# Performance work log

Hardware: AMD Instinct MI355X
Metric: run time of the kernel (lower is better)

Reference implementation:

```python
import jax, jax.numpy as jnp
import numpy as np

B, S, D_IN, D_OUT = 4, 2048, 4096, 11008


def setup_inputs() -> dict:
    key = jax.random.key(0)
    k1, k2, k3 = jax.random.split(key, 3)
    x = jax.random.normal(k1, (B, S, D_IN), dtype=jnp.float32)
    # ternary weights in {-1, 0, +1}, stored as int8 (as the torch buffer does)
    quantized_weight = (jax.random.randint(k2, (D_OUT, D_IN), 0, 3) - 1).astype(jnp.int8)
    weight_scale = jnp.ones((1,), dtype=jnp.float32) * 0.02  # mean-abs scale
    bias = jax.random.normal(k3, (D_OUT,), dtype=jnp.float32) * 0.01
    return {"x": x, "quantized_weight": quantized_weight,
            "weight_scale": weight_scale, "bias": bias}


def reference(x, quantized_weight, weight_scale, bias):
    # Dequantize: ternary int8 -> float, times scalar scale (matches
    # weight = self.quantized_weight.float() * self.weight_scale)
    w = quantized_weight.astype(jnp.float32) * weight_scale[0]
    # F.linear: y = x @ w.T + bias ; x: (B,S,D_in), w: (D_out,D_in)
    out = jnp.einsum("bsd,od->bso", x, w) + bias
    return out
```

## Files before the change

kernel.cpp:

```cpp
#include <hip/hip_runtime.h>
#include <stdint.h>

#define M_DIM 8192
#define N_DIM 11008
#define K_DIM 4096

#define BM 256
#define BN 256
#define BK 128
#define KTILES (K_DIM / BK)

#define FBM 128
#define FBN 128

typedef __attribute__((ext_vector_type(4))) int i32x4;
typedef __attribute__((ext_vector_type(8))) short bf16x8;
typedef __attribute__((ext_vector_type(4))) float f32x4;

__device__ __forceinline__ void async_cp16(const void* g, void* lds_uniform) {
  __builtin_amdgcn_global_load_lds(
      (__attribute__((address_space(1))) void*)(uintptr_t)g,
      (__attribute__((address_space(3))) void*)(uintptr_t)lds_uniform,
      16, 0, 0);
}

__device__ __forceinline__ unsigned short f2bf(float f) {
  unsigned int u = __float_as_uint(f);
  u += 0x7fffu + ((u >> 16) & 1u);
  return (unsigned short)(u >> 16);
}
__device__ __forceinline__ unsigned short i2bf(int v) {
  return (unsigned short)(__float_as_uint((float)v) >> 16);
}

__device__ __forceinline__ int pack4(int a, int b, int c, int d) {
  return (a & 0xFF) | ((b & 0xFF) << 8) | ((c & 0xFF) << 16) | ((d & 0xFF) << 24);
}

__global__ __launch_bounds__(256) void quant_x(const float* __restrict__ x,
                                               signed char* __restrict__ xq,
                                               float* __restrict__ row_step) {
  __shared__ float red[256];
  const unsigned int row = blockIdx.x, t = threadIdx.x;
  const float* xr = x + (size_t)row * K_DIM;
  float4 v[4];
#pragma unroll
  for (int j = 0; j < 4; ++j)
    v[j] = *(const float4*)(xr + j * 1024 + t * 4);

  float m = 0.f;
#pragma unroll
  for (int j = 0; j < 4; ++j) {
    m = fmaxf(m, fmaxf(fmaxf(fabsf(v[j].x), fabsf(v[j].y)),
                       fmaxf(fabsf(v[j].z), fabsf(v[j].w))));
  }
  red[t] = m;
  __syncthreads();
#pragma unroll
  for (int s = 128; s > 0; s >>= 1) {
    if (t < s) red[t] = fmaxf(red[t], red[t + s]);
    __syncthreads();
  }
  const float mx = red[0];
  const float r = (mx > 0.f) ? 127.0f / mx : 0.0f;
  if (t == 0) row_step[row] = (mx > 0.f) ? mx / 127.0f : 0.0f;

  int* out = (int*)(xq + (size_t)row * K_DIM);
#pragma unroll
  for (int j = 0; j < 4; ++j) {
    int q0 = __float2int_rn(v[j].x * r);
    int q1 = __float2int_rn(v[j].y * r);
    int q2 = __float2int_rn(v[j].z * r);
    int q3 = __float2int_rn(v[j].w * r);
    out[j * 256 + t] = pack4(q0, q1, q2, q3);
  }
}

__global__ __launch_bounds__(256) void quant_w(const int4* __restrict__ w,
                                               int* __restrict__ wq) {
  const size_t base = (size_t)blockIdx.x * 1024 + threadIdx.x;
#pragma unroll
  for (int j = 0; j < 4; ++j) {
    int4 a = w[base + j * 256];
    wq[base + j * 256] = pack4(a.x, a.y, a.z, a.w);
  }
}

__device__ __forceinline__ void ktile_iter(
    const signed char* Ab, const signed char* Bb,
    signed char* An, signed char* Bn, bool pf,
    i32x4 (&acc)[8][4],
    const signed char* (&ag)[4], const signed char* (&bg)[4],
    unsigned abase, unsigned bbase, unsigned ldsw)
{
  i32x4 bfr[4][2];
#pragma unroll
  for (int ni = 0; ni < 4; ++ni)
#pragma unroll
    for (int ks = 0; ks < 2; ++ks)
      bfr[ni][ks] = *(const i32x4*)(Bb + ((bbase + ni * 2048u) ^ (unsigned)(ks << 6)));

  i32x4 afr[2][2];

#pragma unroll
  for (int mi = 0; mi < 2; ++mi)
#pragma unroll
    for (int ks = 0; ks < 2; ++ks)
      afr[mi][ks] = *(const i32x4*)(Ab + ((abase + mi * 2048u) ^ (unsigned)(ks << 6)));
  if (pf) {
    async_cp16(ag[0], An + 0 * 8192 + ldsw);
    async_cp16(ag[1], An + 1 * 8192 + ldsw);
    async_cp16(bg[0], Bn + 0 * 8192 + ldsw);
    async_cp16(bg[1], Bn + 1 * 8192 + ldsw);
  }
  __builtin_amdgcn_s_barrier();
  asm volatile("s_waitcnt lgkmcnt(0)" ::: "memory");
  __builtin_amdgcn_sched_barrier(0);
  __builtin_amdgcn_s_setprio(1);
#pragma unroll
  for (int mi = 0; mi < 2; ++mi)
#pragma unroll
    for (int ni = 0; ni < 4; ++ni)
#pragma unroll
      for (int ks = 0; ks < 2; ++ks)
        acc[mi][ni] = __builtin_amdgcn_mfma_i32_16x16x64_i8(afr[mi][ks], bfr[ni][ks], acc[mi][ni], 0, 0, 0);
  __builtin_amdgcn_s_setprio(0);
  __builtin_amdgcn_s_barrier();

#pragma unroll
  for (int mi = 0; mi < 2; ++mi)
#pragma unroll
    for (int ks = 0; ks < 2; ++ks)
      afr[mi][ks] = *(const i32x4*)(Ab + ((abase + (mi + 2) * 2048u) ^ (unsigned)(ks << 6)));
  if (pf) {
    async_cp16(ag[2], An + 2 * 8192 + ldsw);
    async_cp16(ag[3], An + 3 * 8192 + ldsw);
    async_cp16(bg[2], Bn + 2 * 8192 + ldsw);
    async_cp16(bg[3], Bn + 3 * 8192 + ldsw);
  }
  __builtin_amdgcn_s_barrier();
  asm volatile("s_waitcnt lgkmcnt(0)" ::: "memory");
  __builtin_amdgcn_sched_barrier(0);
  __builtin_amdgcn_s_setprio(1);
#pragma unroll
  for (int mi = 0; mi < 2; ++mi)
#pragma unroll
    for (int ni = 0; ni < 4; ++ni)
#pragma unroll
      for (int ks = 0; ks < 2; ++ks)
        acc[mi + 2][ni] = __builtin_amdgcn_mfma_i32_16x16x64_i8(afr[mi][ks], bfr[ni][ks], acc[mi + 2][ni], 0, 0, 0);
  __builtin_amdgcn_s_setprio(0);
  __builtin_amdgcn_s_barrier();

#pragma unroll
  for (int mi = 0; mi < 2; ++mi)
#pragma unroll
    for (int ks = 0; ks < 2; ++ks)
      afr[mi][ks] = *(const i32x4*)(Ab + ((abase + (mi + 4) * 2048u) ^ (unsigned)(ks << 6)));
  __builtin_amdgcn_s_barrier();
  asm volatile("s_waitcnt lgkmcnt(0)" ::: "memory");
  __builtin_amdgcn_sched_barrier(0);
  __builtin_amdgcn_s_setprio(1);
#pragma unroll
  for (int mi = 0; mi < 2; ++mi)
#pragma unroll
    for (int ni = 0; ni < 4; ++ni)
#pragma unroll
      for (int ks = 0; ks < 2; ++ks)
        acc[mi + 4][ni] = __builtin_amdgcn_mfma_i32_16x16x64_i8(afr[mi][ks], bfr[ni][ks], acc[mi + 4][ni], 0, 0, 0);
  __builtin_amdgcn_s_setprio(0);
  __builtin_amdgcn_s_barrier();

#pragma unroll
  for (int mi = 0; mi < 2; ++mi)
#pragma unroll
    for (int ks = 0; ks < 2; ++ks)
      afr[mi][ks] = *(const i32x4*)(Ab + ((abase + (mi + 6) * 2048u) ^ (unsigned)(ks << 6)));
  __builtin_amdgcn_s_barrier();
  asm volatile("s_waitcnt lgkmcnt(0)" ::: "memory");
  __builtin_amdgcn_sched_barrier(0);
  __builtin_amdgcn_s_setprio(1);
#pragma unroll
  for (int mi = 0; mi < 2; ++mi)
#pragma unroll
    for (int ni = 0; ni < 4; ++ni)
#pragma unroll
      for (int ks = 0; ks < 2; ++ks)
        acc[mi + 6][ni] = __builtin_amdgcn_mfma_i32_16x16x64_i8(afr[mi][ks], bfr[ni][ks], acc[mi + 6][ni], 0, 0, 0);
  __builtin_amdgcn_s_setprio(0);
  asm volatile("s_waitcnt vmcnt(0)" ::: "memory");
  __builtin_amdgcn_s_barrier();

#pragma unroll
  for (int g = 0; g < 4; ++g) { ag[g] += BK; bg[g] += BK; }
}

__global__ __launch_bounds__(512, 2) void gemm_i8(
    const signed char* __restrict__ A,
    const signed char* __restrict__ B,
    const float* __restrict__ row_step,
    const float* __restrict__ bias,
    const float* __restrict__ scale_p,
    float* __restrict__ C)
{
  __shared__ __align__(16) signed char As[2][BM * BK];
  __shared__ __align__(16) signed char Bs[2][BN * BK];

  const unsigned t = threadIdx.x;
  const unsigned lane = t & 63u;
  const unsigned wave = t >> 6;
  const unsigned n0 = blockIdx.x * BN;
  const unsigned m0 = blockIdx.y * BM;

  const unsigned wm = (wave >> 2) * 128u;
  const unsigned wn = (wave & 3u) * 64u;
  const unsigned fr = lane & 15u;
  const unsigned fq = lane >> 4;

  const unsigned rst = t >> 3;
  const unsigned cst = (lane & 7u) ^ ((lane >> 3) & 7u);
  const signed char* ag[4];
  const signed char* bg[4];
#pragma unroll
  for (int g = 0; g < 4; ++g) {
    ag[g] = A + (size_t)(m0 + g * 64 + rst) * K_DIM + cst * 16u;
    bg[g] = B + (size_t)(n0 + g * 64 + rst) * K_DIM + cst * 16u;
  }
  const unsigned ldsw = wave * 1024u;

  const unsigned swz = ((fq ^ (fr & 3u)) << 4) | (((fr >> 2) & 1u) << 6);
  const unsigned abase = (wm + fr) * BK + swz;
  const unsigned bbase = (wn + fr) * BK + swz;

  i32x4 acc[8][4];
#pragma unroll
  for (int i = 0; i < 8; ++i)
#pragma unroll
    for (int j = 0; j < 4; ++j)
      acc[i][j] = (i32x4){0, 0, 0, 0};

#pragma unroll
  for (int g = 0; g < 4; ++g) {
    async_cp16(ag[g], As[0] + g * 8192 + ldsw);
    async_cp16(bg[g], Bs[0] + g * 8192 + ldsw);
    ag[g] += BK; bg[g] += BK;
  }
  asm volatile("s_waitcnt vmcnt(0)" ::: "memory");
  __builtin_amdgcn_s_barrier();

  for (int kt = 0; kt < KTILES; kt += 2) {
    ktile_iter(As[0], Bs[0], As[1], Bs[1], true,
               acc, ag, bg, abase, bbase, ldsw);
    ktile_iter(As[1], Bs[1], As[0], Bs[0], (kt + 2) < KTILES,
               acc, ag, bg, abase, bbase, ldsw);
  }

  const float ws = scale_p[0];
  float bb[4];
#pragma unroll
  for (int ni = 0; ni < 4; ++ni)
    bb[ni] = bias[n0 + wn + ni * 16 + fr];

#pragma unroll
  for (int mi = 0; mi < 8; ++mi) {
    const unsigned mg = m0 + wm + mi * 16 + fq * 4;
    const float rs0 = row_step[mg + 0] * ws;
    const float rs1 = row_step[mg + 1] * ws;
    const float rs2 = row_step[mg + 2] * ws;
    const float rs3 = row_step[mg + 3] * ws;
#pragma unroll
    for (int ni = 0; ni < 4; ++ni) {
      const unsigned ng = n0 + wn + ni * 16 + fr;
      i32x4 v = acc[mi][ni];
      float* cp = C + (size_t)mg * N_DIM + ng;
      cp[0]                   = (float)v[0] * rs0 + bb[ni];
      cp[(size_t)1 * N_DIM]   = (float)v[1] * rs1 + bb[ni];
      cp[(size_t)2 * N_DIM]   = (float)v[2] * rs2 + bb[ni];
      cp[(size_t)3 * N_DIM]   = (float)v[3] * rs3 + bb[ni];
    }
  }
}

__global__ __launch_bounds__(256) void gemm_fused(
    const float* __restrict__ X,
    const int* __restrict__ W,
    const float* __restrict__ bias,
    const float* __restrict__ scale_p,
    float* __restrict__ C)
{
  __shared__ __align__(16) unsigned short As[FBM * 32];
  __shared__ __align__(16) unsigned short Bs[FBN * 32];

  const unsigned int t = threadIdx.x;
  const unsigned int n0 = blockIdx.x * FBN;
  const unsigned int m0 = blockIdx.y * FBM;
  const unsigned int lane = t & 63u;
  const unsigned int wave = t >> 6;
  const unsigned int wm = (wave >> 1) * 64u;
  const unsigned int wn = (wave & 1u) * 64u;
  const unsigned int fr = lane & 15u;
  const unsigned int fq = lane >> 4;

  const unsigned short* afp = As + (wm + fr) * 32 + fq * 8u;
  const unsigned short* bfp = Bs + (wn + fr) * 32 + fq * 8u;
  const unsigned int brow = t >> 1, bcol = (t & 1u) * 16u;

  f32x4 acc[4][4];
#pragma unroll
  for (int i = 0; i < 4; ++i)
#pragma unroll
    for (int j = 0; j < 4; ++j)
      acc[i][j] = (f32x4){0.f, 0.f, 0.f, 0.f};

  for (int kt = 0; kt < K_DIM; kt += 32) {
#pragma unroll
    for (int i = 0; i < 4; ++i) {
      unsigned int c = t + i * 256;
      unsigned int row = c >> 3, col = (c & 7u) * 4u;
      float4 v = *(const float4*)(X + (size_t)(m0 + row) * K_DIM + kt + col);
      ushort4 o;
      o.x = f2bf(v.x); o.y = f2bf(v.y); o.z = f2bf(v.z); o.w = f2bf(v.w);
      *(ushort4*)(As + row * 32 + col) = o;
    }
    {
      const int* wp = W + (size_t)(n0 + brow) * K_DIM + kt + bcol;
      int4 a = *(const int4*)(wp);
      int4 b = *(const int4*)(wp + 4);
      int4 c = *(const int4*)(wp + 8);
      int4 d = *(const int4*)(wp + 12);
      uint4 o0, o1;
      o0.x = (unsigned int)i2bf(a.x) | ((unsigned int)i2bf(a.y) << 16);
      o0.y = (unsigned int)i2bf(a.z) | ((unsigned int)i2bf(a.w) << 16);
      o0.z = (unsigned int)i2bf(b.x) | ((unsigned int)i2bf(b.y) << 16);
      o0.w = (unsigned int)i2bf(b.z) | ((unsigned int)i2bf(b.w) << 16);
      o1.x = (unsigned int)i2bf(c.x) | ((unsigned int)i2bf(c.y) << 16);
      o1.y = (unsigned int)i2bf(c.z) | ((unsigned int)i2bf(c.w) << 16);
      o1.z = (unsigned int)i2bf(d.x) | ((unsigned int)i2bf(d.y) << 16);
      o1.w = (unsigned int)i2bf(d.z) | ((unsigned int)i2bf(d.w) << 16);
      *(uint4*)(Bs + brow * 32 + bcol)     = o0;
      *(uint4*)(Bs + brow * 32 + bcol + 8) = o1;
    }
    __syncthreads();

    bf16x8 af[4], bgf[4];
#pragma unroll
    for (int mi = 0; mi < 4; ++mi)
      af[mi] = *(const bf16x8*)(afp + mi * 16 * 32);
#pragma unroll
    for (int ni = 0; ni < 4; ++ni)
      bgf[ni] = *(const bf16x8*)(bfp + ni * 16 * 32);
#pragma unroll
    for (int mi = 0; mi < 4; ++mi)
#pragma unroll
      for (int ni = 0; ni < 4; ++ni)
        acc[mi][ni] = __builtin_amdgcn_mfma_f32_16x16x32_bf16(af[mi], bgf[ni], acc[mi][ni], 0, 0, 0);
    __syncthreads();
  }

  const float scale = scale_p[0];
#pragma unroll
  for (int ni = 0; ni < 4; ++ni) {
    const unsigned int ng = n0 + wn + ni * 16 + fr;
    const float bbv = bias[ng];
#pragma unroll
    for (int mi = 0; mi < 4; ++mi) {
      const unsigned int mg = m0 + wm + mi * 16 + fq * 4;
      f32x4 v = acc[mi][ni];
#pragma unroll
      for (int r = 0; r < 4; ++r)
        C[(size_t)(mg + r) * N_DIM + ng] = v[r] * scale + bbv;
    }
  }
}

extern "C" void kernel_launch(void* const* d_in, const int* in_sizes, int n_in,
                              void* d_out, int out_size, void* d_ws, size_t ws_size,
                              hipStream_t stream) {
  const float* x     = (const float*)d_in[0];
  const int*   wq    = (const int*)d_in[1];
  const float* scale = (const float*)d_in[2];
  const float* bias  = (const float*)d_in[3];
  float* out         = (float*)d_out;

  const size_t xq_bytes = (size_t)M_DIM * K_DIM;
  const size_t wq_bytes = (size_t)N_DIM * K_DIM;
  const size_t rs_bytes = (size_t)M_DIM * sizeof(float);
  const size_t need = xq_bytes + wq_bytes + rs_bytes;

  if (ws_size >= need) {
    signed char* xqp = (signed char*)d_ws;
    signed char* wqp = xqp + xq_bytes;
    float* row_step  = (float*)(wqp + wq_bytes);

    dim3 grid(N_DIM / BN, M_DIM / BM);
    quant_x<<<M_DIM, 256, 0, stream>>>(x, xqp, row_step);
    quant_w<<<(unsigned)(wq_bytes / (16 * 256)), 256, 0, stream>>>(
        (const int4*)wq, (int*)wqp);
    gemm_i8<<<grid, 512, 0, stream>>>(xqp, wqp, row_step, bias, scale, out);
  } else {
    dim3 fgrid(N_DIM / FBN, M_DIM / FBM);
    gemm_fused<<<fgrid, 256, 0, stream>>>(x, wq, bias, scale, out);
  }
}
```

Baseline: 903.6 us.

## Shrink int8 GEMM tiles, raise occupancy, add XCD block remap and nontemporal stores

Reduces the int8 GEMM block tile from 256x256x128 to 256x128x64, with each of 8 waves computing a 64x64 sub-tile. The LDS XOR swizzle and global-to-LDS copy mapping are reworked to match, and launch bounds now ask for 4 blocks per CU. The aim is more resident blocks to hide latency, and fewer registers because the accumulator is half the size. Block ids are remapped so neighbouring tiles are grouped per XCD, which should improve L2 reuse. Output stores become nontemporal. The trade-offs are lower arithmetic intensity per block and twice as many k-iterations with barriers. LDS demand may also still cap occupancy below the requested 4 blocks.

```diff
diff --git a/kernel.cpp b/kernel.cpp
--- a/kernel.cpp
+++ b/kernel.cpp
@@ -6,8 +6,8 @@
 #define K_DIM 4096
 
 #define BM 256
-#define BN 256
-#define BK 128
+#define BN 128
+#define BK 64
 #define KTILES (K_DIM / BK)
 
 #define FBM 128
@@ -89,29 +89,24 @@
 __device__ __forceinline__ void ktile_iter(
     const signed char* Ab, const signed char* Bb,
     signed char* An, signed char* Bn, bool pf,
-    i32x4 (&acc)[8][4],
-    const signed char* (&ag)[4], const signed char* (&bg)[4],
+    i32x4 (&acc)[4][4],
+    const signed char*& ag0, const signed char*& ag1, const signed char*& bg0,
     unsigned abase, unsigned bbase, unsigned ldsw)
 {
-  i32x4 bfr[4][2];
+  i32x4 bfr[4];
 #pragma unroll
   for (int ni = 0; ni < 4; ++ni)
-#pragma unroll
-    for (int ks = 0; ks < 2; ++ks)
-      bfr[ni][ks] = *(const i32x4*)(Bb + ((bbase + ni * 2048u) ^ (unsigned)(ks << 6)));
-
-  i32x4 afr[2][2];
+    bfr[ni] = *(const i32x4*)(Bb + bbase + ni * 1024u);
+
+  i32x4 afr[2];
 
 #pragma unroll
   for (int mi = 0; mi < 2; ++mi)
-#pragma unroll
-    for (int ks = 0; ks < 2; ++ks)
-      afr[mi][ks] = *(const i32x4*)(Ab + ((abase + mi * 2048u) ^ (unsigned)(ks << 6)));
+    afr[mi] = *(const i32x4*)(Ab + abase + mi * 1024u);
   if (pf) {
-    async_cp16(ag[0], An + 0 * 8192 + ldsw);
-    async_cp16(ag[1], An + 1 * 8192 + ldsw);
-    async_cp16(bg[0], Bn + 0 * 8192 + ldsw);
-    async_cp16(bg[1], Bn + 1 * 8192 + ldsw);
+    async_cp16(ag0, An + ldsw);
+    async_cp16(ag1, An + 8192 + ldsw);
+    async_cp16(bg0, Bn + ldsw);
   }
   __builtin_amdgcn_s_barrier();
   asm volatile("s_waitcnt lgkmcnt(0)" ::: "memory");
@@ -121,23 +116,13 @@
   for (int mi = 0; mi < 2; ++mi)
 #pragma unroll
     for (int ni = 0; ni < 4; ++ni)
-#pragma unroll
-      for (int ks = 0; ks < 2; ++ks)
-        acc[mi][ni] = __builtin_amdgcn_mfma_i32_16x16x64_i8(afr[mi][ks], bfr[ni][ks], acc[mi][ni], 0, 0, 0);
+      acc[mi][ni] = __builtin_amdgcn_mfma_i32_16x16x64_i8(afr[mi], bfr[ni], acc[mi][ni], 0, 0, 0);
   __builtin_amdgcn_s_setprio(0);
   __builtin_amdgcn_s_barrier();
 
 #pragma unroll
   for (int mi = 0; mi < 2; ++mi)
-#pragma unroll
-    for (int ks = 0; ks < 2; ++ks)
-      afr[mi][ks] = *(const i32x4*)(Ab + ((abase + (mi + 2) * 2048u) ^ (unsigned)(ks << 6)));
-  if (pf) {
-    async_cp16(ag[2], An + 2 * 8192 + ldsw);
-    async_cp16(ag[3], An + 3 * 8192 + ldsw);
-    async_cp16(bg[2], Bn + 2 * 8192 + ldsw);
-    async_cp16(bg[3], Bn + 3 * 8192 + ldsw);
-  }
+    afr[mi] = *(const i32x4*)(Ab + abase + (mi + 2) * 1024u);
   __builtin_amdgcn_s_barrier();
   asm volatile("s_waitcnt lgkmcnt(0)" ::: "memory");
   __builtin_amdgcn_sched_barrier(0);
@@ -146,56 +131,15 @@
   for (int mi = 0; mi < 2; ++mi)
 #pragma unroll
     for (int ni = 0; ni < 4; ++ni)
-#pragma unroll
-      for (int ks = 0; ks < 2; ++ks)
-        acc[mi + 2][ni] = __builtin_amdgcn_mfma_i32_16x16x64_i8(afr[mi][ks], bfr[ni][ks], acc[mi + 2][ni], 0, 0, 0);
-  __builtin_amdgcn_s_setprio(0);
-  __builtin_amdgcn_s_barrier();
-
-#pragma unroll
-  for (int mi = 0; mi < 2; ++mi)
-#pragma unroll
-    for (int ks = 0; ks < 2; ++ks)
-      afr[mi][ks] = *(const i32x4*)(Ab + ((abase + (mi + 4) * 2048u) ^ (unsigned)(ks << 6)));
-  __builtin_amdgcn_s_barrier();
-  asm volatile("s_waitcnt lgkmcnt(0)" ::: "memory");
-  __builtin_amdgcn_sched_barrier(0);
-  __builtin_amdgcn_s_setprio(1);
-#pragma unroll
-  for (int mi = 0; mi < 2; ++mi)
-#pragma unroll
-    for (int ni = 0; ni < 4; ++ni)
-#pragma unroll
-      for (int ks = 0; ks < 2; ++ks)
-        acc[mi + 4][ni] = __builtin_amdgcn_mfma_i32_16x16x64_i8(afr[mi][ks], bfr[ni][ks], acc[mi + 4][ni], 0, 0, 0);
-  __builtin_amdgcn_s_setprio(0);
-  __builtin_amdgcn_s_barrier();
-
-#pragma unroll
-  for (int mi = 0; mi < 2; ++mi)
-#pragma unroll
-    for (int ks = 0; ks < 2; ++ks)
-      afr[mi][ks] = *(const i32x4*)(Ab + ((abase + (mi + 6) * 2048u) ^ (unsigned)(ks << 6)));
-  __builtin_amdgcn_s_barrier();
-  asm volatile("s_waitcnt lgkmcnt(0)" ::: "memory");
-  __builtin_amdgcn_sched_barrier(0);
-  __builtin_amdgcn_s_setprio(1);
-#pragma unroll
-  for (int mi = 0; mi < 2; ++mi)
-#pragma unroll
-    for (int ni = 0; ni < 4; ++ni)
-#pragma unroll
-      for (int ks = 0; ks < 2; ++ks)
-        acc[mi + 6][ni] = __builtin_amdgcn_mfma_i32_16x16x64_i8(afr[mi][ks], bfr[ni][ks], acc[mi + 6][ni], 0, 0, 0);
+      acc[mi + 2][ni] = __builtin_amdgcn_mfma_i32_16x16x64_i8(afr[mi], bfr[ni], acc[mi + 2][ni], 0, 0, 0);
   __builtin_amdgcn_s_setprio(0);
   asm volatile("s_waitcnt vmcnt(0)" ::: "memory");
   __builtin_amdgcn_s_barrier();
 
-#pragma unroll
-  for (int g = 0; g < 4; ++g) { ag[g] += BK; bg[g] += BK; }
-}
-
-__global__ __launch_bounds__(512, 2) void gemm_i8(
+  ag0 += BK; ag1 += BK; bg0 += BK;
+}
+
+__global__ __launch_bounds__(512, 4) void gemm_i8(
     const signed char* __restrict__ A,
     const signed char* __restrict__ B,
     const float* __restrict__ row_step,
@@ -209,50 +153,49 @@
   const unsigned t = threadIdx.x;
   const unsigned lane = t & 63u;
   const unsigned wave = t >> 6;
-  const unsigned n0 = blockIdx.x * BN;
-  const unsigned m0 = blockIdx.y * BM;
-
-  const unsigned wm = (wave >> 2) * 128u;
-  const unsigned wn = (wave & 3u) * 64u;
+
+  const unsigned nbx = gridDim.x;
+  unsigned bid = blockIdx.y * nbx + blockIdx.x;
+  const unsigned cpx = (nbx * gridDim.y) >> 3;
+  bid = (bid & 7u) * cpx + (bid >> 3);
+  const unsigned n0 = (bid % nbx) * BN;
+  const unsigned m0 = (bid / nbx) * BM;
+
+  const unsigned wm = (wave >> 1) * 64u;
+  const unsigned wn = (wave & 1u) * 64u;
   const unsigned fr = lane & 15u;
   const unsigned fq = lane >> 4;
 
-  const unsigned rst = t >> 3;
-  const unsigned cst = (lane & 7u) ^ ((lane >> 3) & 7u);
-  const signed char* ag[4];
-  const signed char* bg[4];
-#pragma unroll
-  for (int g = 0; g < 4; ++g) {
-    ag[g] = A + (size_t)(m0 + g * 64 + rst) * K_DIM + cst * 16u;
-    bg[g] = B + (size_t)(n0 + g * 64 + rst) * K_DIM + cst * 16u;
-  }
-  const unsigned ldsw = wave * 1024u;
-
-  const unsigned swz = ((fq ^ (fr & 3u)) << 4) | (((fr >> 2) & 1u) << 6);
+  const unsigned rst = t >> 2;
+  const unsigned c_src = (t & 3u) ^ ((t >> 2) & 3u) ^ ((t >> 4) & 3u);
+  const signed char* ag0 = A + (size_t)(m0 + rst) * K_DIM + c_src * 16u;
+  const signed char* ag1 = A + (size_t)(m0 + 128 + rst) * K_DIM + c_src * 16u;
+  const signed char* bg0 = B + (size_t)(n0 + rst) * K_DIM + c_src * 16u;
+  const unsigned ldsw = (t & 448u) * 16u;
+
+  const unsigned swz = (fq ^ (fr & 3u) ^ (fr >> 2)) << 4;
   const unsigned abase = (wm + fr) * BK + swz;
   const unsigned bbase = (wn + fr) * BK + swz;
 
-  i32x4 acc[8][4];
-#pragma unroll
-  for (int i = 0; i < 8; ++i)
+  i32x4 acc[4][4];
+#pragma unroll
+  for (int i = 0; i < 4; ++i)
 #pragma unroll
     for (int j = 0; j < 4; ++j)
       acc[i][j] = (i32x4){0, 0, 0, 0};
 
-#pragma unroll
-  for (int g = 0; g < 4; ++g) {
-    async_cp16(ag[g], As[0] + g * 8192 + ldsw);
-    async_cp16(bg[g], Bs[0] + g * 8192 + ldsw);
-    ag[g] += BK; bg[g] += BK;
-  }
+  async_cp16(ag0, As[0] + ldsw);
+  async_cp16(ag1, As[0] + 8192 + ldsw);
+  async_cp16(bg0, Bs[0] + ldsw);
+  ag0 += BK; ag1 += BK; bg0 += BK;
   asm volatile("s_waitcnt vmcnt(0)" ::: "memory");
   __builtin_amdgcn_s_barrier();
 
   for (int kt = 0; kt < KTILES; kt += 2) {
     ktile_iter(As[0], Bs[0], As[1], Bs[1], true,
-               acc, ag, bg, abase, bbase, ldsw);
+               acc, ag0, ag1, bg0, abase, bbase, ldsw);
     ktile_iter(As[1], Bs[1], As[0], Bs[0], (kt + 2) < KTILES,
-               acc, ag, bg, abase, bbase, ldsw);
+               acc, ag0, ag1, bg0, abase, bbase, ldsw);
   }
 
   const float ws = scale_p[0];
@@ -262,7 +205,7 @@
     bb[ni] = bias[n0 + wn + ni * 16 + fr];
 
 #pragma unroll
-  for (int mi = 0; mi < 8; ++mi) {
+  for (int mi = 0; mi < 4; ++mi) {
     const unsigned mg = m0 + wm + mi * 16 + fq * 4;
     const float rs0 = row_step[mg + 0] * ws;
     const float rs1 = row_step[mg + 1] * ws;
@@ -273,10 +216,10 @@
       const unsigned ng = n0 + wn + ni * 16 + fr;
       i32x4 v = acc[mi][ni];
       float* cp = C + (size_t)mg * N_DIM + ng;
-      cp[0]                   = (float)v[0] * rs0 + bb[ni];
-      cp[(size_t)1 * N_DIM]   = (float)v[1] * rs1 + bb[ni];
-      cp[(size_t)2 * N_DIM]   = (float)v[2] * rs2 + bb[ni];
-      cp[(size_t)3 * N_DIM]   = (float)v[3] * rs3 + bb[ni];
+      __builtin_nontemporal_store((float)v[0] * rs0 + bb[ni], cp);
+      __builtin_nontemporal_store((float)v[1] * rs1 + bb[ni], cp + (size_t)1 * N_DIM);
+      __builtin_nontemporal_store((float)v[2] * rs2 + bb[ni], cp + (size_t)2 * N_DIM);
+      __builtin_nontemporal_store((float)v[3] * rs3 + bb[ni], cp + (size_t)3 * N_DIM);
     }
   }
 }
```

New measurement: 921.7 us. +2.0%, slower.
